# Kernel optimization log

Measured on AMD Instinct MI355X. Metric: run time of the kernel, lower is better.

## Reference

```python
import jax, jax.numpy as jnp
import numpy as np

T, D, E, K = 8192, 4096, 64, 8


def setup_inputs() -> dict:
    key = jax.random.key(0)
    k1, k2, k3, k4 = jax.random.split(key, 4)
    x = jax.random.normal(k1, (T, D), dtype=jnp.float32)
    # nn.Linear stores weight as [out_features, in_features]
    Wg = jax.random.normal(k2, (E, D), dtype=jnp.float32) * (1.0 / np.sqrt(D))
    Wc = jax.random.normal(k3, (E, D), dtype=jnp.float32) * (1.0 / np.sqrt(D))
    extra_scale = jnp.zeros((E,), dtype=jnp.float32)  # init zeros as in module
    extra_bias = jax.random.normal(k4, (E,), dtype=jnp.float32) * 0.01
    return {"x": x, "Wg": Wg, "Wc": Wc, "extra_scale": extra_scale,
            "extra_bias": extra_bias, "topk": K}


def reference(x, Wg, Wc, extra_scale, extra_bias, topk):
    # scores = |classifier(x) * silu(gate(x))|, softmax in fp32
    gate = jnp.einsum('td,ed->te', x, Wg)        # [T, E]
    cls = jnp.einsum('td,ed->te', x, Wc)         # [T, E]
    scores = jnp.abs(cls * jax.nn.silu(gate))
    scores = jax.nn.softmax(scores.astype(jnp.float32), axis=-1)
    biased = scores + extra_bias[None, :]        # load-balance bias, used only for selection
    _, indices = jax.lax.top_k(biased, topk)     # [T, K]
    original = 1.0 + scores * extra_scale[None, :]
    weights = jnp.take_along_axis(original, indices, axis=1)  # [T, K]
    return weights.astype(x.dtype), indices
```

## Files before the change

kernel.cpp:

```cpp
#include <hip/hip_runtime.h>
#include <math.h>


#define T_DIM 8192
#define D_DIM 4096
#define E_DIM 64
#define N2    128
#define KTOP  8
#define MB_ROWS 32

typedef __attribute__((ext_vector_type(8)))  short bfrag8;
typedef __attribute__((ext_vector_type(16))) float f32x16;

__device__ __forceinline__ unsigned short f2bf_rne(float f) {
    unsigned int u = __float_as_uint(f);
    unsigned int r = u + 0x7fffu + ((u >> 16) & 1u);
    return (unsigned short)(r >> 16);
}
__device__ __forceinline__ float bf2f(unsigned short h) {
    return __uint_as_float(((unsigned int)h) << 16);
}
__device__ __forceinline__ void split3(float v, unsigned short& h,
                                       unsigned short& m, unsigned short& l) {
    h = f2bf_rne(v);
    const float r1 = v - bf2f(h);
    m = f2bf_rne(r1);
    const float r2 = r1 - bf2f(m);
    l = f2bf_rne(r2);
}

__global__ __launch_bounds__(256)
void router_prep(const float* __restrict__ Wg, const float* __restrict__ Wc,
                 unsigned short* __restrict__ Wpk)
{
    const int t   = blockIdx.x * 256 + threadIdx.x;
    const int col = t >> 9;
    const int ch  = t & 511;
    const int k   = ch << 3;

    const float* src = (col < E_DIM) ? (Wg + (size_t)col * D_DIM)
                                     : (Wc + (size_t)(col - E_DIM) * D_DIM);
    const float4 w0 = ((const float4*)(src + k))[0];
    const float4 w1 = ((const float4*)(src + k))[1];
    const float v[8] = {w0.x, w0.y, w0.z, w0.w, w1.x, w1.y, w1.z, w1.w};

    unsigned short hv[8], mv[8], lv[8];
    #pragma unroll
    for (int j = 0; j < 8; ++j) split3(v[j], hv[j], mv[j], lv[j]);

    const int k32 = k >> 5, h2 = (k >> 4) & 1, lh = (k >> 3) & 1;
    const int n = col >> 5, lane = lh * 32 + (col & 31);
    const size_t base = ((((size_t)k32 * 4 + n) * 3 + 0) * 2 + h2) * 512 + (size_t)lane * 8;
    *(ushort4*)(Wpk + base)          = make_ushort4(hv[0], hv[1], hv[2], hv[3]);
    *(ushort4*)(Wpk + base + 4)      = make_ushort4(hv[4], hv[5], hv[6], hv[7]);
    *(ushort4*)(Wpk + base + 1024)   = make_ushort4(mv[0], mv[1], mv[2], mv[3]);
    *(ushort4*)(Wpk + base + 1028)   = make_ushort4(mv[4], mv[5], mv[6], mv[7]);
    *(ushort4*)(Wpk + base + 2048)   = make_ushort4(lv[0], lv[1], lv[2], lv[3]);
    *(ushort4*)(Wpk + base + 2052)   = make_ushort4(lv[4], lv[5], lv[6], lv[7]);
}

__global__ __launch_bounds__(256, 4)
void router_gemm(const float* __restrict__ x,
                 const unsigned short* __restrict__ Wpk,
                 float* __restrict__ P,
                 int sliceK)
{
    __shared__ unsigned short sF[2][3][2][64][8];

    const int tid  = threadIdx.x;
    const int lane = tid & 63;
    const int wc   = tid >> 6;
    const int l31  = lane & 31;
    const int lh   = lane >> 5;
    const int mb   = blockIdx.x;
    const int ks   = blockIdx.y;
    const int k0   = ks * sliceK;
    const int NT   = sliceK >> 5;
    const int brow0 = mb * MB_ROWS;

    const int srow = tid >> 3;
    const int kq   = tid & 7;
    const int h2w  = kq >> 2;
    const int lew  = ((kq >> 1) & 1) * 32 + srow;
    const int jw   = (kq & 1) * 4;
    const float* gsrc = x + (size_t)(brow0 + srow) * D_DIM + kq * 4;

    f32x16 acc;
    #pragma unroll
    for (int r = 0; r < 16; ++r) acc[r] = 0.f;

    #define WRITE_TILE(v_, bf_)                                                  \
        {                                                                        \
            ushort4 hv_, mv_, lv_;                                               \
            unsigned short h_, m_, l_;                                           \
            split3((v_).x, h_, m_, l_); hv_.x = h_; mv_.x = m_; lv_.x = l_;      \
            split3((v_).y, h_, m_, l_); hv_.y = h_; mv_.y = m_; lv_.y = l_;      \
            split3((v_).z, h_, m_, l_); hv_.z = h_; mv_.z = m_; lv_.z = l_;      \
            split3((v_).w, h_, m_, l_); hv_.w = h_; mv_.w = m_; lv_.w = l_;      \
            *(ushort4*)&sF[bf_][0][h2w][lew][jw] = hv_;                          \
            *(ushort4*)&sF[bf_][1][h2w][lew][jw] = mv_;                          \
            *(ushort4*)&sF[bf_][2][h2w][lew][jw] = lv_;                          \
        }

    {
        const float4 v0 = *(const float4*)(gsrc + k0);
        WRITE_TILE(v0, 0);
    }
    __syncthreads();

    for (int t = 0; t < NT; ++t) {
        const int bf = t & 1;
        const bool more = (t + 1 < NT);

        float4 nx;
        if (more) nx = *(const float4*)(gsrc + k0 + (t + 1) * 32);

        bfrag8 ah[2], am[2], al[2];
        #pragma unroll
        for (int h2 = 0; h2 < 2; ++h2) {
            ah[h2] = *(const bfrag8*)&sF[bf][0][h2][lane][0];
            am[h2] = *(const bfrag8*)&sF[bf][1][h2][lane][0];
            al[h2] = *(const bfrag8*)&sF[bf][2][h2][lane][0];
        }

        const size_t k32 = (size_t)((k0 + t * 32) >> 5);
        #pragma unroll
        for (int h2 = 0; h2 < 2; ++h2) {
            const unsigned short* bb =
                Wpk + ((((k32 * 4 + wc) * 3 + 0) * 2 + h2) * 64 + lane) * 8;
            const bfrag8 bh = *(const bfrag8*)(bb);
            const bfrag8 bm = *(const bfrag8*)(bb + 1024);
            const bfrag8 bl = *(const bfrag8*)(bb + 2048);
            acc = __builtin_amdgcn_mfma_f32_32x32x16_bf16(ah[h2], bl, acc, 0, 0, 0);
            acc = __builtin_amdgcn_mfma_f32_32x32x16_bf16(al[h2], bh, acc, 0, 0, 0);
            acc = __builtin_amdgcn_mfma_f32_32x32x16_bf16(am[h2], bm, acc, 0, 0, 0);
            acc = __builtin_amdgcn_mfma_f32_32x32x16_bf16(ah[h2], bm, acc, 0, 0, 0);
            acc = __builtin_amdgcn_mfma_f32_32x32x16_bf16(am[h2], bh, acc, 0, 0, 0);
            acc = __builtin_amdgcn_mfma_f32_32x32x16_bf16(ah[h2], bh, acc, 0, 0, 0);
        }

        if (more) WRITE_TILE(nx, bf ^ 1);
        __syncthreads();
    }
    #undef WRITE_TILE

    float* Pb = P + ((size_t)ks * T_DIM + brow0) * N2 + wc * 32 + l31;
    #pragma unroll
    for (int r = 0; r < 16; ++r) {
        const int wrow = (r & 3) + 8 * (r >> 2) + 4 * lh;
        Pb[(size_t)wrow * N2] = acc[r];
    }
}

__global__ __launch_bounds__(256)
void router_topk(const float* __restrict__ P,
                 const float* __restrict__ scale,
                 const float* __restrict__ bias,
                 float* __restrict__ out,
                 int ksplit)
{
    const int lane = threadIdx.x & 63;
    const int wid  = threadIdx.x >> 6;
    const int row  = blockIdx.x * 4 + wid;

    float g = 0.f, c = 0.f;
    for (int ks = 0; ks < ksplit; ++ks) {
        const float* p = P + ((size_t)ks * T_DIM + row) * N2;
        g += p[lane];
        c += p[E_DIM + lane];
    }
    const float sg = g / (1.f + expf(-g));
    const float v  = fabsf(c * sg);

    float m = v;
    #pragma unroll
    for (int off = 32; off >= 1; off >>= 1) m = fmaxf(m, __shfl_xor(m, off));
    const float e = expf(v - m);
    float Z = e;
    #pragma unroll
    for (int off = 32; off >= 1; off >>= 1) Z += __shfl_xor(Z, off);
    const float s = e / Z;

    const float sc  = scale[lane];
    float cur = s + bias[lane];

    float myw = 0.f; int myi = 0;
    #pragma unroll
    for (int j = 0; j < KTOP; ++j) {
        float bv = cur; int bi = lane;
        #pragma unroll
        for (int off = 32; off >= 1; off >>= 1) {
            const float ov = __shfl_xor(bv, off);
            const int   oi = __shfl_xor(bi, off);
            if (ov > bv || (ov == bv && oi < bi)) { bv = ov; bi = oi; }
        }
        const float s_bi  = __shfl(s,  bi);
        const float sc_bi = __shfl(sc, bi);
        const float w = 1.f + s_bi * sc_bi;
        if (lane == j)  { myw = w; myi = bi; }
        if (lane == bi) cur = -INFINITY;
    }

    if (lane < KTOP) {
        out[(size_t)row * KTOP + lane] = myw;
        out[(size_t)T_DIM * KTOP + (size_t)row * KTOP + lane] = (float)myi;
    }
}

extern "C" void kernel_launch(void* const* d_in, const int* in_sizes, int n_in,
                              void* d_out, int out_size, void* d_ws, size_t ws_size,
                              hipStream_t stream)
{
    const float* x  = (const float*)d_in[0];
    const float* Wg = (const float*)d_in[1];
    const float* Wc = (const float*)d_in[2];
    const float* sc = (const float*)d_in[3];
    const float* bs = (const float*)d_in[4];
    float* out = (float*)d_out;
    float* P   = (float*)d_ws;

    const size_t PER = (size_t)T_DIM * N2 * sizeof(float);
    const size_t WSP = (size_t)N2 * D_DIM * sizeof(unsigned short);

    int S = 8;
    while (S > 1 && (size_t)S * PER + 3 * WSP > ws_size) S >>= 1;
    const int sliceK = D_DIM / S;

    unsigned short* Wpk = (unsigned short*)((char*)d_ws + (size_t)S * PER);

    router_prep<<<256, 256, 0, stream>>>(Wg, Wc, Wpk);
    router_gemm<<<dim3(T_DIM / MB_ROWS, S), 256, 0, stream>>>(x, Wpk, P, sliceK);
    router_topk<<<T_DIM / 4, 256, 0, stream>>>(P, sc, bs, out, S);
}
```

Before: 265.7 us.

## Double row tile per block, prefetch x two steps ahead, pad LDS

Each GEMM block now covers 64 token rows in two 32-row groups, so every B fragment of the packed weights loaded from global memory feeds twice as many MFMAs. The x prefetch is deepened to two k-steps ahead using nontemporal loads. The LDS planes are padded to reduce bank conflicts, and __syncthreads is replaced by an explicit lgkmcnt wait plus s_barrier. Output stores are nontemporal. The cost is more accumulator registers and halving the number of blocks, which may hurt occupancy, since launch bounds still request 4 blocks per CU.

```diff
diff --git a/kernel.cpp b/kernel.cpp
--- a/kernel.cpp
+++ b/kernel.cpp
@@ -7,10 +7,16 @@
 #define E_DIM 64
 #define N2    128
 #define KTOP  8
-#define MB_ROWS 32
+#define MB_ROWS 64
+
+#define LDS_H2S 512
+#define LDS_PS  1040
+#define LDS_RGS (3 * LDS_PS)
+#define LDS_BFS (2 * LDS_RGS)
 
 typedef __attribute__((ext_vector_type(8)))  short bfrag8;
 typedef __attribute__((ext_vector_type(16))) float f32x16;
+typedef __attribute__((ext_vector_type(4)))  float f4;
 
 __device__ __forceinline__ unsigned short f2bf_rne(float f) {
     unsigned int u = __float_as_uint(f);
@@ -65,7 +71,7 @@
                  float* __restrict__ P,
                  int sliceK)
 {
-    __shared__ unsigned short sF[2][3][2][64][8];
+    __shared__ unsigned short sF[2 * LDS_BFS];
 
     const int tid  = threadIdx.x;
     const int lane = tid & 63;
@@ -83,13 +89,17 @@
     const int h2w  = kq >> 2;
     const int lew  = ((kq >> 1) & 1) * 32 + srow;
     const int jw   = (kq & 1) * 4;
-    const float* gsrc = x + (size_t)(brow0 + srow) * D_DIM + kq * 4;
-
-    f32x16 acc;
-    #pragma unroll
-    for (int r = 0; r < 16; ++r) acc[r] = 0.f;
-
-    #define WRITE_TILE(v_, bf_)                                                  \
+    const int wbase = h2w * LDS_H2S + lew * 8 + jw;
+    const float* gsrc0 = x + (size_t)(brow0 + srow) * D_DIM + k0 + kq * 4;
+    const float* gsrc1 = gsrc0 + (size_t)32 * D_DIM;
+
+    f32x16 acc[2];
+    #pragma unroll
+    for (int rg = 0; rg < 2; ++rg)
+        #pragma unroll
+        for (int r = 0; r < 16; ++r) acc[rg][r] = 0.f;
+
+    #define WRITE_HALF(v_, bf_, rg_)                                             \
         {                                                                        \
             ushort4 hv_, mv_, lv_;                                               \
             unsigned short h_, m_, l_;                                           \
@@ -97,30 +107,34 @@
             split3((v_).y, h_, m_, l_); hv_.y = h_; mv_.y = m_; lv_.y = l_;      \
             split3((v_).z, h_, m_, l_); hv_.z = h_; mv_.z = m_; lv_.z = l_;      \
             split3((v_).w, h_, m_, l_); hv_.w = h_; mv_.w = m_; lv_.w = l_;      \
-            *(ushort4*)&sF[bf_][0][h2w][lew][jw] = hv_;                          \
-            *(ushort4*)&sF[bf_][1][h2w][lew][jw] = mv_;                          \
-            *(ushort4*)&sF[bf_][2][h2w][lew][jw] = lv_;                          \
+            const int o_ = (bf_) * LDS_BFS + (rg_) * LDS_RGS + wbase;            \
+            *(ushort4*)&sF[o_]              = hv_;                               \
+            *(ushort4*)&sF[o_ + LDS_PS]     = mv_;                               \
+            *(ushort4*)&sF[o_ + 2 * LDS_PS] = lv_;                               \
         }
 
     {
-        const float4 v0 = *(const float4*)(gsrc + k0);
-        WRITE_TILE(v0, 0);
-    }
-    __syncthreads();
+        const f4 v0 = __builtin_nontemporal_load((const f4*)gsrc0);
+        const f4 v1 = __builtin_nontemporal_load((const f4*)gsrc1);
+        WRITE_HALF(v0, 0, 0);
+        WRITE_HALF(v1, 0, 1);
+    }
+    f4 xa0 = {0,0,0,0}, xa1 = {0,0,0,0};
+    f4 xb0 = {0,0,0,0}, xb1 = {0,0,0,0};
+    if (NT > 1) {
+        xa0 = __builtin_nontemporal_load((const f4*)(gsrc0 + 32));
+        xa1 = __builtin_nontemporal_load((const f4*)(gsrc1 + 32));
+    }
+    asm volatile("s_waitcnt lgkmcnt(0)" ::: "memory");
+    __builtin_amdgcn_s_barrier();
 
     for (int t = 0; t < NT; ++t) {
         const int bf = t & 1;
-        const bool more = (t + 1 < NT);
-
-        float4 nx;
-        if (more) nx = *(const float4*)(gsrc + k0 + (t + 1) * 32);
-
-        bfrag8 ah[2], am[2], al[2];
-        #pragma unroll
-        for (int h2 = 0; h2 < 2; ++h2) {
-            ah[h2] = *(const bfrag8*)&sF[bf][0][h2][lane][0];
-            am[h2] = *(const bfrag8*)&sF[bf][1][h2][lane][0];
-            al[h2] = *(const bfrag8*)&sF[bf][2][h2][lane][0];
+        const int fbase = bf * LDS_BFS;
+
+        if (t + 2 < NT) {
+            xb0 = __builtin_nontemporal_load((const f4*)(gsrc0 + (t + 2) * 32));
+            xb1 = __builtin_nontemporal_load((const f4*)(gsrc1 + (t + 2) * 32));
         }
 
         const size_t k32 = (size_t)((k0 + t * 32) >> 5);
@@ -131,24 +145,39 @@
             const bfrag8 bh = *(const bfrag8*)(bb);
             const bfrag8 bm = *(const bfrag8*)(bb + 1024);
             const bfrag8 bl = *(const bfrag8*)(bb + 2048);
-            acc = __builtin_amdgcn_mfma_f32_32x32x16_bf16(ah[h2], bl, acc, 0, 0, 0);
-            acc = __builtin_amdgcn_mfma_f32_32x32x16_bf16(al[h2], bh, acc, 0, 0, 0);
-            acc = __builtin_amdgcn_mfma_f32_32x32x16_bf16(am[h2], bm, acc, 0, 0, 0);
-            acc = __builtin_amdgcn_mfma_f32_32x32x16_bf16(ah[h2], bm, acc, 0, 0, 0);
-            acc = __builtin_amdgcn_mfma_f32_32x32x16_bf16(am[h2], bh, acc, 0, 0, 0);
-            acc = __builtin_amdgcn_mfma_f32_32x32x16_bf16(ah[h2], bh, acc, 0, 0, 0);
-        }
-
-        if (more) WRITE_TILE(nx, bf ^ 1);
-        __syncthreads();
-    }
-    #undef WRITE_TILE
-
-    float* Pb = P + ((size_t)ks * T_DIM + brow0) * N2 + wc * 32 + l31;
-    #pragma unroll
-    for (int r = 0; r < 16; ++r) {
-        const int wrow = (r & 3) + 8 * (r >> 2) + 4 * lh;
-        Pb[(size_t)wrow * N2] = acc[r];
+            #pragma unroll
+            for (int rg = 0; rg < 2; ++rg) {
+                const int ab = fbase + rg * LDS_RGS + h2 * LDS_H2S + lane * 8;
+                const bfrag8 ah = *(const bfrag8*)&sF[ab];
+                const bfrag8 am = *(const bfrag8*)&sF[ab + LDS_PS];
+                const bfrag8 al = *(const bfrag8*)&sF[ab + 2 * LDS_PS];
+                acc[rg] = __builtin_amdgcn_mfma_f32_32x32x16_bf16(ah, bl, acc[rg], 0, 0, 0);
+                acc[rg] = __builtin_amdgcn_mfma_f32_32x32x16_bf16(al, bh, acc[rg], 0, 0, 0);
+                acc[rg] = __builtin_amdgcn_mfma_f32_32x32x16_bf16(am, bm, acc[rg], 0, 0, 0);
+                acc[rg] = __builtin_amdgcn_mfma_f32_32x32x16_bf16(ah, bm, acc[rg], 0, 0, 0);
+                acc[rg] = __builtin_amdgcn_mfma_f32_32x32x16_bf16(am, bh, acc[rg], 0, 0, 0);
+                acc[rg] = __builtin_amdgcn_mfma_f32_32x32x16_bf16(ah, bh, acc[rg], 0, 0, 0);
+            }
+        }
+
+        if (t + 1 < NT) {
+            WRITE_HALF(xa0, bf ^ 1, 0);
+            WRITE_HALF(xa1, bf ^ 1, 1);
+        }
+        asm volatile("s_waitcnt lgkmcnt(0)" ::: "memory");
+        __builtin_amdgcn_s_barrier();
+        xa0 = xb0; xa1 = xb1;
+    }
+    #undef WRITE_HALF
+
+    #pragma unroll
+    for (int rg = 0; rg < 2; ++rg) {
+        float* Pb = P + ((size_t)ks * T_DIM + brow0 + rg * 32) * N2 + wc * 32 + l31;
+        #pragma unroll
+        for (int r = 0; r < 16; ++r) {
+            const int wrow = (r & 3) + 8 * (r >> 2) + 4 * lh;
+            __builtin_nontemporal_store(acc[rg][r], &Pb[(size_t)wrow * N2]);
+        }
     }
 }
 
```

New measurement: 249.0 us. 1.07x faster.

## Double GEMM block rows to 64 with 512 threads, pad LDS, nontemporal IO

Applied to the files above, without the earlier changes.

Each GEMM block now covers 64 token rows using 8 waves, two row groups sharing each B-fragment column slice. This halves the number of blocks and the repeated global loads of the packed weights per row. The LDS planes are padded to reduce bank conflicts. __syncthreads is replaced with an explicit lgkmcnt wait plus s_barrier, and loads of x and stores of P use nontemporal hints. B fragments are loaded before the A reads to overlap latency. The costs are higher register and LDS use per block, and a launch bound of 8 may constrain registers.

```diff
diff --git a/kernel.cpp b/kernel.cpp
--- a/kernel.cpp
+++ b/kernel.cpp
@@ -7,10 +7,16 @@
 #define E_DIM 64
 #define N2    128
 #define KTOP  8
-#define MB_ROWS 32
+#define MB_ROWS 64
+
+#define LDS_H2S 512
+#define LDS_PS  1040
+#define LDS_RGS (3 * LDS_PS)
+#define LDS_BFS (2 * LDS_RGS)
 
 typedef __attribute__((ext_vector_type(8)))  short bfrag8;
 typedef __attribute__((ext_vector_type(16))) float f32x16;
+typedef __attribute__((ext_vector_type(4)))  float f4;
 
 __device__ __forceinline__ unsigned short f2bf_rne(float f) {
     unsigned int u = __float_as_uint(f);
@@ -59,17 +65,19 @@
     *(ushort4*)(Wpk + base + 2052)   = make_ushort4(lv[4], lv[5], lv[6], lv[7]);
 }
 
-__global__ __launch_bounds__(256, 4)
+__global__ __launch_bounds__(512, 8)
 void router_gemm(const float* __restrict__ x,
                  const unsigned short* __restrict__ Wpk,
                  float* __restrict__ P,
                  int sliceK)
 {
-    __shared__ unsigned short sF[2][3][2][64][8];
+    __shared__ unsigned short sF[2 * LDS_BFS];
 
     const int tid  = threadIdx.x;
     const int lane = tid & 63;
-    const int wc   = tid >> 6;
+    const int wid  = tid >> 6;
+    const int rg   = wid >> 2;
+    const int wc   = wid & 3;
     const int l31  = lane & 31;
     const int lh   = lane >> 5;
     const int mb   = blockIdx.x;
@@ -80,16 +88,18 @@
 
     const int srow = tid >> 3;
     const int kq   = tid & 7;
+    const int rgs  = srow >> 5;
     const int h2w  = kq >> 2;
-    const int lew  = ((kq >> 1) & 1) * 32 + srow;
+    const int lew  = ((kq >> 1) & 1) * 32 + (srow & 31);
     const int jw   = (kq & 1) * 4;
-    const float* gsrc = x + (size_t)(brow0 + srow) * D_DIM + kq * 4;
+    const int wbase = rgs * LDS_RGS + h2w * LDS_H2S + lew * 8 + jw;
+    const float* gsrc = x + (size_t)(brow0 + srow) * D_DIM + k0 + kq * 4;
 
     f32x16 acc;
     #pragma unroll
     for (int r = 0; r < 16; ++r) acc[r] = 0.f;
 
-    #define WRITE_TILE(v_, bf_)                                                  \
+    #define WRITE_ONE(v_, bf_)                                                   \
         {                                                                        \
             ushort4 hv_, mv_, lv_;                                               \
             unsigned short h_, m_, l_;                                           \
@@ -97,58 +107,74 @@
             split3((v_).y, h_, m_, l_); hv_.y = h_; mv_.y = m_; lv_.y = l_;      \
             split3((v_).z, h_, m_, l_); hv_.z = h_; mv_.z = m_; lv_.z = l_;      \
             split3((v_).w, h_, m_, l_); hv_.w = h_; mv_.w = m_; lv_.w = l_;      \
-            *(ushort4*)&sF[bf_][0][h2w][lew][jw] = hv_;                          \
-            *(ushort4*)&sF[bf_][1][h2w][lew][jw] = mv_;                          \
-            *(ushort4*)&sF[bf_][2][h2w][lew][jw] = lv_;                          \
+            const int o_ = (bf_) * LDS_BFS + wbase;                              \
+            *(ushort4*)&sF[o_]              = hv_;                               \
+            *(ushort4*)&sF[o_ + LDS_PS]     = mv_;                               \
+            *(ushort4*)&sF[o_ + 2 * LDS_PS] = lv_;                               \
         }
 
     {
-        const float4 v0 = *(const float4*)(gsrc + k0);
-        WRITE_TILE(v0, 0);
-    }
-    __syncthreads();
+        const f4 v0 = __builtin_nontemporal_load((const f4*)gsrc);
+        WRITE_ONE(v0, 0);
+    }
+    asm volatile("s_waitcnt lgkmcnt(0)" ::: "memory");
+    __builtin_amdgcn_s_barrier();
 
     for (int t = 0; t < NT; ++t) {
         const int bf = t & 1;
+        const int fbase = bf * LDS_BFS + rg * LDS_RGS;
+        const size_t k32 = (size_t)((k0 + t * 32) >> 5);
         const bool more = (t + 1 < NT);
 
-        float4 nx;
-        if (more) nx = *(const float4*)(gsrc + k0 + (t + 1) * 32);
-
-        bfrag8 ah[2], am[2], al[2];
-        #pragma unroll
-        for (int h2 = 0; h2 < 2; ++h2) {
-            ah[h2] = *(const bfrag8*)&sF[bf][0][h2][lane][0];
-            am[h2] = *(const bfrag8*)&sF[bf][1][h2][lane][0];
-            al[h2] = *(const bfrag8*)&sF[bf][2][h2][lane][0];
-        }
-
-        const size_t k32 = (size_t)((k0 + t * 32) >> 5);
-        #pragma unroll
-        for (int h2 = 0; h2 < 2; ++h2) {
-            const unsigned short* bb =
-                Wpk + ((((k32 * 4 + wc) * 3 + 0) * 2 + h2) * 64 + lane) * 8;
-            const bfrag8 bh = *(const bfrag8*)(bb);
-            const bfrag8 bm = *(const bfrag8*)(bb + 1024);
-            const bfrag8 bl = *(const bfrag8*)(bb + 2048);
-            acc = __builtin_amdgcn_mfma_f32_32x32x16_bf16(ah[h2], bl, acc, 0, 0, 0);
-            acc = __builtin_amdgcn_mfma_f32_32x32x16_bf16(al[h2], bh, acc, 0, 0, 0);
-            acc = __builtin_amdgcn_mfma_f32_32x32x16_bf16(am[h2], bm, acc, 0, 0, 0);
-            acc = __builtin_amdgcn_mfma_f32_32x32x16_bf16(ah[h2], bm, acc, 0, 0, 0);
-            acc = __builtin_amdgcn_mfma_f32_32x32x16_bf16(am[h2], bh, acc, 0, 0, 0);
-            acc = __builtin_amdgcn_mfma_f32_32x32x16_bf16(ah[h2], bh, acc, 0, 0, 0);
-        }
-
-        if (more) WRITE_TILE(nx, bf ^ 1);
-        __syncthreads();
-    }
-    #undef WRITE_TILE
-
-    float* Pb = P + ((size_t)ks * T_DIM + brow0) * N2 + wc * 32 + l31;
+        const unsigned short* bb0 =
+            Wpk + ((((k32 * 4 + wc) * 3 + 0) * 2 + 0) * 64 + lane) * 8;
+        const bfrag8 bh0 = *(const bfrag8*)(bb0);
+        const bfrag8 bm0 = *(const bfrag8*)(bb0 + 1024);
+        const bfrag8 bl0 = *(const bfrag8*)(bb0 + 2048);
+        const unsigned short* bb1 = bb0 + 512;
+        const bfrag8 BH1 = *(const bfrag8*)(bb1);
+        const bfrag8 BM1 = *(const bfrag8*)(bb1 + 1024);
+        const bfrag8 BL1 = *(const bfrag8*)(bb1 + 2048);
+
+        f4 xa;
+        if (more) xa = __builtin_nontemporal_load((const f4*)(gsrc + (t + 1) * 32));
+
+        {
+            const int ab0 = fbase + 0 * LDS_H2S + lane * 8;
+            const bfrag8 ah = *(const bfrag8*)&sF[ab0];
+            const bfrag8 am = *(const bfrag8*)&sF[ab0 + LDS_PS];
+            const bfrag8 al = *(const bfrag8*)&sF[ab0 + 2 * LDS_PS];
+            acc = __builtin_amdgcn_mfma_f32_32x32x16_bf16(ah, bl0, acc, 0, 0, 0);
+            acc = __builtin_amdgcn_mfma_f32_32x32x16_bf16(al, bh0, acc, 0, 0, 0);
+            acc = __builtin_amdgcn_mfma_f32_32x32x16_bf16(am, bm0, acc, 0, 0, 0);
+            acc = __builtin_amdgcn_mfma_f32_32x32x16_bf16(ah, bm0, acc, 0, 0, 0);
+            acc = __builtin_amdgcn_mfma_f32_32x32x16_bf16(am, bh0, acc, 0, 0, 0);
+            acc = __builtin_amdgcn_mfma_f32_32x32x16_bf16(ah, bh0, acc, 0, 0, 0);
+        }
+        {
+            const int ab1 = fbase + 1 * LDS_H2S + lane * 8;
+            const bfrag8 ah = *(const bfrag8*)&sF[ab1];
+            const bfrag8 am = *(const bfrag8*)&sF[ab1 + LDS_PS];
+            const bfrag8 al = *(const bfrag8*)&sF[ab1 + 2 * LDS_PS];
+            acc = __builtin_amdgcn_mfma_f32_32x32x16_bf16(ah, BL1, acc, 0, 0, 0);
+            acc = __builtin_amdgcn_mfma_f32_32x32x16_bf16(al, BH1, acc, 0, 0, 0);
+            acc = __builtin_amdgcn_mfma_f32_32x32x16_bf16(am, BM1, acc, 0, 0, 0);
+            acc = __builtin_amdgcn_mfma_f32_32x32x16_bf16(ah, BM1, acc, 0, 0, 0);
+            acc = __builtin_amdgcn_mfma_f32_32x32x16_bf16(am, BH1, acc, 0, 0, 0);
+            acc = __builtin_amdgcn_mfma_f32_32x32x16_bf16(ah, BH1, acc, 0, 0, 0);
+        }
+
+        if (more) WRITE_ONE(xa, bf ^ 1);
+        asm volatile("s_waitcnt lgkmcnt(0)" ::: "memory");
+        __builtin_amdgcn_s_barrier();
+    }
+    #undef WRITE_ONE
+
+    float* Pb = P + ((size_t)ks * T_DIM + brow0 + rg * 32) * N2 + wc * 32 + l31;
     #pragma unroll
     for (int r = 0; r < 16; ++r) {
         const int wrow = (r & 3) + 8 * (r >> 2) + 4 * lh;
-        Pb[(size_t)wrow * N2] = acc[r];
+        __builtin_nontemporal_store(acc[r], &Pb[(size_t)wrow * N2]);
     }
 }
 
@@ -229,6 +255,6 @@
     unsigned short* Wpk = (unsigned short*)((char*)d_ws + (size_t)S * PER);
 
     router_prep<<<256, 256, 0, stream>>>(Wg, Wc, Wpk);
-    router_gemm<<<dim3(T_DIM / MB_ROWS, S), 256, 0, stream>>>(x, Wpk, P, sliceK);
+    router_gemm<<<dim3(T_DIM / MB_ROWS, S), 512, 0, stream>>>(x, Wpk, P, sliceK);
     router_topk<<<T_DIM / 4, 256, 0, stream>>>(P, sc, bs, out, S);
 }
```

New measurement: 254.8 us. 1.04x faster.

## Enlarge GEMM row tile to 128 rows with padded LDS and B-fragment reuse

Applied to the files above, without the earlier changes.

Each router_gemm block now covers 128 token rows in four 32-row groups, so every wave reuses the weight fragments it loads from global memory across four accumulators instead of one. The LDS tile is rebuilt as a flat, padded array to cut bank conflicts. x is loaded with nontemporal 64-byte-per-thread loads and P is written with nontemporal stores, and MFMA priority is raised around the compute section. The cost is more registers and LDS per block, so occupancy drops to 2 blocks per CU, and the grid has 4x fewer row blocks.

```diff
diff --git a/kernel.cpp b/kernel.cpp
--- a/kernel.cpp
+++ b/kernel.cpp
@@ -7,10 +7,17 @@
 #define E_DIM 64
 #define N2    128
 #define KTOP  8
-#define MB_ROWS 32
+#define MB_ROWS 128
+
+#define LDS_H2S 520
+#define LDS_PS  1056
+#define LDS_RGS (3 * LDS_PS)
+#define LDS_BFS (4 * LDS_RGS)
 
 typedef __attribute__((ext_vector_type(8)))  short bfrag8;
+typedef __attribute__((ext_vector_type(8)))  unsigned short us8;
 typedef __attribute__((ext_vector_type(16))) float f32x16;
+typedef __attribute__((ext_vector_type(4)))  float f4;
 
 __device__ __forceinline__ unsigned short f2bf_rne(float f) {
     unsigned int u = __float_as_uint(f);
@@ -59,13 +66,13 @@
     *(ushort4*)(Wpk + base + 2052)   = make_ushort4(lv[4], lv[5], lv[6], lv[7]);
 }
 
-__global__ __launch_bounds__(256, 4)
+__global__ __launch_bounds__(256, 2)
 void router_gemm(const float* __restrict__ x,
                  const unsigned short* __restrict__ Wpk,
                  float* __restrict__ P,
                  int sliceK)
 {
-    __shared__ unsigned short sF[2][3][2][64][8];
+    __shared__ unsigned short sF[2 * LDS_BFS];
 
     const int tid  = threadIdx.x;
     const int lane = tid & 63;
@@ -78,77 +85,107 @@
     const int NT   = sliceK >> 5;
     const int brow0 = mb * MB_ROWS;
 
-    const int srow = tid >> 3;
-    const int kq   = tid & 7;
-    const int h2w  = kq >> 2;
-    const int lew  = ((kq >> 1) & 1) * 32 + srow;
-    const int jw   = (kq & 1) * 4;
-    const float* gsrc = x + (size_t)(brow0 + srow) * D_DIM + kq * 4;
-
-    f32x16 acc;
-    #pragma unroll
-    for (int r = 0; r < 16; ++r) acc[r] = 0.f;
-
-    #define WRITE_TILE(v_, bf_)                                                  \
+    const int srow = tid >> 1;
+    const int seg  = tid & 1;
+    const int wbase = (srow >> 5) * LDS_RGS + seg * LDS_H2S + (srow & 31) * 8;
+    const float* gsrc = x + (size_t)(brow0 + srow) * D_DIM + k0 + seg * 16;
+
+    f32x16 acc[4];
+    #pragma unroll
+    for (int rg = 0; rg < 4; ++rg)
+        #pragma unroll
+        for (int r = 0; r < 16; ++r) acc[rg][r] = 0.f;
+
+    #define WRITE_TILE(bf_)                                                      \
         {                                                                        \
-            ushort4 hv_, mv_, lv_;                                               \
-            unsigned short h_, m_, l_;                                           \
-            split3((v_).x, h_, m_, l_); hv_.x = h_; mv_.x = m_; lv_.x = l_;      \
-            split3((v_).y, h_, m_, l_); hv_.y = h_; mv_.y = m_; lv_.y = l_;      \
-            split3((v_).z, h_, m_, l_); hv_.z = h_; mv_.z = m_; lv_.z = l_;      \
-            split3((v_).w, h_, m_, l_); hv_.w = h_; mv_.w = m_; lv_.w = l_;      \
-            *(ushort4*)&sF[bf_][0][h2w][lew][jw] = hv_;                          \
-            *(ushort4*)&sF[bf_][1][h2w][lew][jw] = mv_;                          \
-            *(ushort4*)&sF[bf_][2][h2w][lew][jw] = lv_;                          \
-        }
-
-    {
-        const float4 v0 = *(const float4*)(gsrc + k0);
-        WRITE_TILE(v0, 0);
-    }
-    __syncthreads();
+            const float fv[16] = {c0.x,c0.y,c0.z,c0.w, c1.x,c1.y,c1.z,c1.w,      \
+                                  c2.x,c2.y,c2.z,c2.w, c3.x,c3.y,c3.z,c3.w};     \
+            _Pragma("unroll")                                                    \
+            for (int lh_ = 0; lh_ < 2; ++lh_) {                                  \
+                us8 hv_, mv_, lv_;                                               \
+                _Pragma("unroll")                                                \
+                for (int j_ = 0; j_ < 8; ++j_) {                                 \
+                    unsigned short h_, m_, l_;                                   \
+                    split3(fv[lh_ * 8 + j_], h_, m_, l_);                        \
+                    hv_[j_] = h_; mv_[j_] = m_; lv_[j_] = l_;                    \
+                }                                                                \
+                const int o_ = (bf_) * LDS_BFS + wbase + lh_ * 256;              \
+                *(us8*)&sF[o_]              = hv_;                               \
+                *(us8*)&sF[o_ + LDS_PS]     = mv_;                               \
+                *(us8*)&sF[o_ + 2 * LDS_PS] = lv_;                               \
+            }                                                                    \
+        }
+
+    f4 c0, c1, c2, c3;
+    c0 = __builtin_nontemporal_load((const f4*)(gsrc));
+    c1 = __builtin_nontemporal_load((const f4*)(gsrc + 4));
+    c2 = __builtin_nontemporal_load((const f4*)(gsrc + 8));
+    c3 = __builtin_nontemporal_load((const f4*)(gsrc + 12));
+    WRITE_TILE(0);
+    asm volatile("s_waitcnt lgkmcnt(0)" ::: "memory");
+    __builtin_amdgcn_s_barrier();
 
     for (int t = 0; t < NT; ++t) {
         const int bf = t & 1;
+        const size_t k32 = (size_t)((k0 + t * 32) >> 5);
         const bool more = (t + 1 < NT);
 
-        float4 nx;
-        if (more) nx = *(const float4*)(gsrc + k0 + (t + 1) * 32);
-
-        bfrag8 ah[2], am[2], al[2];
-        #pragma unroll
-        for (int h2 = 0; h2 < 2; ++h2) {
-            ah[h2] = *(const bfrag8*)&sF[bf][0][h2][lane][0];
-            am[h2] = *(const bfrag8*)&sF[bf][1][h2][lane][0];
-            al[h2] = *(const bfrag8*)&sF[bf][2][h2][lane][0];
-        }
-
-        const size_t k32 = (size_t)((k0 + t * 32) >> 5);
-        #pragma unroll
-        for (int h2 = 0; h2 < 2; ++h2) {
-            const unsigned short* bb =
-                Wpk + ((((k32 * 4 + wc) * 3 + 0) * 2 + h2) * 64 + lane) * 8;
-            const bfrag8 bh = *(const bfrag8*)(bb);
-            const bfrag8 bm = *(const bfrag8*)(bb + 1024);
-            const bfrag8 bl = *(const bfrag8*)(bb + 2048);
-            acc = __builtin_amdgcn_mfma_f32_32x32x16_bf16(ah[h2], bl, acc, 0, 0, 0);
-            acc = __builtin_amdgcn_mfma_f32_32x32x16_bf16(al[h2], bh, acc, 0, 0, 0);
-            acc = __builtin_amdgcn_mfma_f32_32x32x16_bf16(am[h2], bm, acc, 0, 0, 0);
-            acc = __builtin_amdgcn_mfma_f32_32x32x16_bf16(ah[h2], bm, acc, 0, 0, 0);
-            acc = __builtin_amdgcn_mfma_f32_32x32x16_bf16(am[h2], bh, acc, 0, 0, 0);
-            acc = __builtin_amdgcn_mfma_f32_32x32x16_bf16(ah[h2], bh, acc, 0, 0, 0);
-        }
-
-        if (more) WRITE_TILE(nx, bf ^ 1);
-        __syncthreads();
+        const unsigned short* bb =
+            Wpk + (((k32 * 4 + wc) * 3) * 2 * 64 + (size_t)lane) * 8;
+        const bfrag8 bh0 = *(const bfrag8*)(bb);
+        const bfrag8 bm0 = *(const bfrag8*)(bb + 1024);
+        const bfrag8 bl0 = *(const bfrag8*)(bb + 2048);
+        const bfrag8 bh1 = *(const bfrag8*)(bb + 512);
+        const bfrag8 bm1 = *(const bfrag8*)(bb + 1536);
+        const bfrag8 bl1 = *(const bfrag8*)(bb + 2560);
+
+        if (more) {
+            const float* gp = gsrc + (t + 1) * 32;
+            c0 = __builtin_nontemporal_load((const f4*)(gp));
+            c1 = __builtin_nontemporal_load((const f4*)(gp + 4));
+            c2 = __builtin_nontemporal_load((const f4*)(gp + 8));
+            c3 = __builtin_nontemporal_load((const f4*)(gp + 12));
+        }
+
+        __builtin_amdgcn_s_setprio(1);
+        #pragma unroll
+        for (int rg = 0; rg < 4; ++rg) {
+            const int ab = bf * LDS_BFS + rg * LDS_RGS + lane * 8;
+            const bfrag8 ah0 = *(const bfrag8*)&sF[ab];
+            const bfrag8 am0 = *(const bfrag8*)&sF[ab + LDS_PS];
+            const bfrag8 al0 = *(const bfrag8*)&sF[ab + 2 * LDS_PS];
+            const bfrag8 ah1 = *(const bfrag8*)&sF[ab + LDS_H2S];
+            const bfrag8 am1 = *(const bfrag8*)&sF[ab + LDS_H2S + LDS_PS];
+            const bfrag8 al1 = *(const bfrag8*)&sF[ab + LDS_H2S + 2 * LDS_PS];
+            acc[rg] = __builtin_amdgcn_mfma_f32_32x32x16_bf16(ah0, bl0, acc[rg], 0, 0, 0);
+            acc[rg] = __builtin_amdgcn_mfma_f32_32x32x16_bf16(al0, bh0, acc[rg], 0, 0, 0);
+            acc[rg] = __builtin_amdgcn_mfma_f32_32x32x16_bf16(am0, bm0, acc[rg], 0, 0, 0);
+            acc[rg] = __builtin_amdgcn_mfma_f32_32x32x16_bf16(ah0, bm0, acc[rg], 0, 0, 0);
+            acc[rg] = __builtin_amdgcn_mfma_f32_32x32x16_bf16(am0, bh0, acc[rg], 0, 0, 0);
+            acc[rg] = __builtin_amdgcn_mfma_f32_32x32x16_bf16(ah0, bh0, acc[rg], 0, 0, 0);
+            acc[rg] = __builtin_amdgcn_mfma_f32_32x32x16_bf16(ah1, bl1, acc[rg], 0, 0, 0);
+            acc[rg] = __builtin_amdgcn_mfma_f32_32x32x16_bf16(al1, bh1, acc[rg], 0, 0, 0);
+            acc[rg] = __builtin_amdgcn_mfma_f32_32x32x16_bf16(am1, bm1, acc[rg], 0, 0, 0);
+            acc[rg] = __builtin_amdgcn_mfma_f32_32x32x16_bf16(ah1, bm1, acc[rg], 0, 0, 0);
+            acc[rg] = __builtin_amdgcn_mfma_f32_32x32x16_bf16(am1, bh1, acc[rg], 0, 0, 0);
+            acc[rg] = __builtin_amdgcn_mfma_f32_32x32x16_bf16(ah1, bh1, acc[rg], 0, 0, 0);
+        }
+        __builtin_amdgcn_s_setprio(0);
+
+        if (more) WRITE_TILE(bf ^ 1);
+        asm volatile("s_waitcnt lgkmcnt(0)" ::: "memory");
+        __builtin_amdgcn_s_barrier();
     }
     #undef WRITE_TILE
 
-    float* Pb = P + ((size_t)ks * T_DIM + brow0) * N2 + wc * 32 + l31;
-    #pragma unroll
-    for (int r = 0; r < 16; ++r) {
-        const int wrow = (r & 3) + 8 * (r >> 2) + 4 * lh;
-        Pb[(size_t)wrow * N2] = acc[r];
+    #pragma unroll
+    for (int rg = 0; rg < 4; ++rg) {
+        float* Pb = P + ((size_t)ks * T_DIM + brow0 + rg * 32) * N2 + wc * 32 + l31;
+        #pragma unroll
+        for (int r = 0; r < 16; ++r) {
+            const int wrow = (r & 3) + 8 * (r >> 2) + 4 * lh;
+            __builtin_nontemporal_store(acc[rg][r], &Pb[(size_t)wrow * N2]);
+        }
     }
 }
 
```

Measured after the change: 257.1 us. -3.2%, faster.
